# Performance work log

Measured on AMD Instinct MI355X. Metric: run time of the kernel, lower is better.

## Reference

```python
import jax, jax.numpy as jnp
import numpy as np

B, S, H, NH = 2, 2048, 1024, 16
HD = H // NH
INV_NORM = 1.0 / float(np.sqrt(HD))
BETA = 1.0


def setup_inputs() -> dict:
    key = jax.random.key(0)
    ks = jax.random.split(key, 8)
    causal = ~jnp.tril(jnp.ones((S, S), dtype=bool))  # True = masked (future)
    return {
        "hidden_states": jax.random.normal(ks[0], (B, S, H), dtype=jnp.float32),
        "residual": jax.random.normal(ks[1], (B, S, H), dtype=jnp.float32),
        "alibi": jax.random.normal(ks[2], (B * NH, 1, S), dtype=jnp.float32) * 0.1,
        "attention_mask": jnp.broadcast_to(causal[None, None], (B, 1, S, S)),
        "W_qkv": jax.random.normal(ks[3], (3 * H, H), dtype=jnp.float32) * (1.0 / np.sqrt(H)),
        "b_qkv": jax.random.normal(ks[4], (3 * H,), dtype=jnp.float32) * 0.02,
        "W_d": jax.random.normal(ks[5], (H, H), dtype=jnp.float32) * (1.0 / np.sqrt(H)),
        "b_d": jax.random.normal(ks[6], (H,), dtype=jnp.float32) * 0.02,
    }


def reference(hidden_states, residual, alibi, attention_mask, W_qkv, b_qkv, W_d, b_d):
    b, s, h = hidden_states.shape
    # fused QKV projection, split per-head interleaved [B,S,NH,3,HD]
    fused = hidden_states @ W_qkv.T + b_qkv
    fused = fused.reshape(b, s, NH, 3, HD)
    q = jnp.transpose(fused[..., 0, :], (0, 2, 1, 3))  # [B,NH,S,HD]
    k = jnp.transpose(fused[..., 1, :], (0, 2, 1, 3))
    v = jnp.transpose(fused[..., 2, :], (0, 2, 1, 3))
    # baddbmm: beta*alibi + alpha * q @ k^T
    scores = BETA * alibi.reshape(b, NH, 1, s) + INV_NORM * jnp.einsum(
        "bhqd,bhkd->bhqk", q, k
    )  # [B,NH,S,S]
    neg_min = jnp.finfo(scores.dtype).min
    scores = jnp.where(attention_mask, neg_min, scores)
    probs = jax.nn.softmax(scores.astype(jnp.float32), axis=-1).astype(scores.dtype)
    ctx = jnp.einsum("bhqk,bhkd->bhqd", probs, v)  # [B,NH,S,HD]
    ctx = jnp.transpose(ctx, (0, 2, 1, 3)).reshape(b, s, h)  # merge heads
    out = ctx @ W_d.T + b_d
    return residual + out  # dropout p=0
```

## Files before the change

kernel.cpp:

```cpp
#include <hip/hip_runtime.h>
#include <stdint.h>

#define BATCH 2
#define SLEN 2048
#define HDIM 1024
#define NH 16
#define HD 64
#define NHEADS 32
#define M_ROWS 4096
#define N_QKV 3072

typedef float f32x4 __attribute__((ext_vector_type(4)));
typedef float f32x16 __attribute__((ext_vector_type(16)));
typedef short bf16x8 __attribute__((ext_vector_type(8)));

typedef __attribute__((address_space(1))) unsigned int GU32;
typedef __attribute__((address_space(3))) unsigned int LU32;

__device__ __forceinline__ void gld16(const void* g, void* l) {
  __builtin_amdgcn_global_load_lds((GU32*)g, (LU32*)l, 16, 0, 0);
}

__device__ __forceinline__ unsigned short f2bf(float x) {
  union { float f; unsigned int u; } v; v.f = x;
  unsigned int r = v.u + 0x7fffu + ((v.u >> 16) & 1u);
  return (unsigned short)(r >> 16);
}

__device__ __forceinline__ float fexp2(float x) {
  float r; asm("v_exp_f32 %0, %1" : "=v"(r) : "v"(x)); return r;
}
__device__ __forceinline__ unsigned cvtpk(float lo, float hi) {
  unsigned r; asm("v_cvt_pk_bf16_f32 %0, %1, %2" : "=v"(r) : "v"(lo), "v"(hi)); return r;
}

#define MFMA32(a, b, c) __builtin_amdgcn_mfma_f32_32x32x16_bf16(a, b, c, 0, 0, 0)
#define MFMA16(a, b, c) __builtin_amdgcn_mfma_f32_16x16x32_bf16(a, b, c, 0, 0, 0)
#define ZERO16 {0.f,0.f,0.f,0.f,0.f,0.f,0.f,0.f,0.f,0.f,0.f,0.f,0.f,0.f,0.f,0.f}

__global__ void __launch_bounds__(256) k_prep(
    const float* __restrict__ hidden, const float* __restrict__ wqkv,
    const float* __restrict__ wd,
    unsigned short* __restrict__ hb, unsigned short* __restrict__ wqkb,
    unsigned short* __restrict__ wdb) {
  int bid = blockIdx.x;
  const float* src;
  unsigned short* dst;
  int i;
  if (bid < 4096)      { src = hidden; dst = hb;   i = bid * 256 + threadIdx.x; }
  else if (bid < 7168) { src = wqkv;  dst = wqkb;  i = (bid - 4096) * 256 + threadIdx.x; }
  else                 { src = wd;    dst = wdb;   i = (bid - 7168) * 256 + threadIdx.x; }
  float4 v = ((const float4*)src)[i];
  ushort4 o;
  o.x = f2bf(v.x); o.y = f2bf(v.y); o.z = f2bf(v.z); o.w = f2bf(v.w);
  ((ushort4*)dst)[i] = o;
}

__global__ void __launch_bounds__(256) k_gemm_qkv(
    const unsigned short* __restrict__ A,
    const unsigned short* __restrict__ Bw,
    const float* __restrict__ bias,
    unsigned short* __restrict__ Qo,
    unsigned short* __restrict__ Ko,
    unsigned short* __restrict__ Vto) {
  __shared__ __align__(16) unsigned short Alds[128 * 32];
  __shared__ __align__(16) unsigned short Blds[128 * 32];
  const int tid = threadIdx.x;
  const int w = tid >> 6, lane = tid & 63;
  const int g = lane >> 4, l15 = lane & 15;
  const int wr = w >> 1, wc = w & 1;
  const int tm = blockIdx.x * 128, tn = blockIdx.y * 128;

  const f32x4 zero = {0.f, 0.f, 0.f, 0.f};
  f32x4 acc[4][4];
#pragma unroll
  for (int m = 0; m < 4; ++m)
#pragma unroll
    for (int n = 0; n < 4; ++n) acc[m][n] = zero;

  for (int k0 = 0; k0 < 1024; k0 += 32) {
    __syncthreads();
#pragma unroll
    for (int r = 0; r < 2; ++r) {
      int c = r * 256 + w * 64 + lane;
      int row = c >> 2, cc = c & 3;
      gld16(A + (size_t)(tm + row) * 1024 + k0 + cc * 8,
            (char*)Alds + (r * 256 + w * 64) * 16);
      gld16(Bw + (size_t)(tn + row) * 1024 + k0 + cc * 8,
            (char*)Blds + (r * 256 + w * 64) * 16);
    }
    __syncthreads();
    bf16x8 af[4], bfv[4];
#pragma unroll
    for (int m = 0; m < 4; ++m)
      af[m] = *(const bf16x8*)(Alds + (wr * 64 + m * 16 + l15) * 32 + g * 8);
#pragma unroll
    for (int n = 0; n < 4; ++n)
      bfv[n] = *(const bf16x8*)(Blds + (wc * 64 + n * 16 + l15) * 32 + g * 8);
#pragma unroll
    for (int m = 0; m < 4; ++m)
#pragma unroll
      for (int n = 0; n < 4; ++n)
        acc[m][n] = MFMA16(af[m], bfv[n], acc[m][n]);
  }

#pragma unroll
  for (int n = 0; n < 4; ++n) {
    int col = tn + wc * 64 + n * 16 + l15;
    float bv = bias[col];
    int c6 = col >> 6;
    int nh = c6 / 3;
    int which = c6 - nh * 3;
    int hd = col & 63;
#pragma unroll
    for (int m = 0; m < 4; ++m) {
      int row0 = tm + wr * 64 + m * 16 + g * 4;
      int b = row0 >> 11;
      int s0 = row0 & 2047;
      int head = b * NH + nh;
      if (which == 2) {
        ushort4 pk;
        pk.x = f2bf(acc[m][n][0] + bv);
        pk.y = f2bf(acc[m][n][1] + bv);
        pk.z = f2bf(acc[m][n][2] + bv);
        pk.w = f2bf(acc[m][n][3] + bv);
        *(ushort4*)(Vto + ((size_t)head * HD + hd) * SLEN + s0) = pk;
      } else {
        unsigned short* dst = (which == 0) ? Qo : Ko;
        size_t base = (size_t)head * SLEN * HD;
#pragma unroll
        for (int j = 0; j < 4; ++j)
          dst[base + (size_t)(s0 + j) * HD + hd] = f2bf(acc[m][n][j] + bv);
      }
    }
  }
}

__global__ void __launch_bounds__(256) k_gemm_out(
    const unsigned short* __restrict__ A,
    const unsigned short* __restrict__ Bw,
    const float* __restrict__ bias,
    const float* __restrict__ residual,
    float* __restrict__ out) {
  __shared__ __align__(16) unsigned short Alds[128 * 32];
  __shared__ __align__(16) unsigned short Blds[64 * 32];
  const int tid = threadIdx.x;
  const int w = tid >> 6, lane = tid & 63;
  const int g = lane >> 4, l15 = lane & 15;
  const int wr = w >> 1, wc = w & 1;
  const int tm = blockIdx.x * 128, tn = blockIdx.y * 64;

  const f32x4 zero = {0.f, 0.f, 0.f, 0.f};
  f32x4 acc[4][2];
#pragma unroll
  for (int m = 0; m < 4; ++m)
#pragma unroll
    for (int n = 0; n < 2; ++n) acc[m][n] = zero;

  for (int k0 = 0; k0 < 1024; k0 += 32) {
    __syncthreads();
#pragma unroll
    for (int r = 0; r < 2; ++r) {
      int c = r * 256 + tid;
      int row = c >> 2, cc = c & 3;
      gld16(A + (size_t)(tm + row) * 1024 + k0 + cc * 8,
            (char*)Alds + c * 16);
    }
    {
      int row = tid >> 2, cc = tid & 3;
      gld16(Bw + (size_t)(tn + row) * 1024 + k0 + cc * 8,
            (char*)Blds + tid * 16);
    }
    __syncthreads();
    bf16x8 af[4], bfv[2];
#pragma unroll
    for (int m = 0; m < 4; ++m)
      af[m] = *(const bf16x8*)(Alds + (wr * 64 + m * 16 + l15) * 32 + g * 8);
#pragma unroll
    for (int n = 0; n < 2; ++n)
      bfv[n] = *(const bf16x8*)(Blds + (wc * 32 + n * 16 + l15) * 32 + g * 8);
#pragma unroll
    for (int m = 0; m < 4; ++m)
#pragma unroll
      for (int n = 0; n < 2; ++n)
        acc[m][n] = MFMA16(af[m], bfv[n], acc[m][n]);
  }

#pragma unroll
  for (int n = 0; n < 2; ++n) {
    int col = tn + wc * 32 + n * 16 + l15;
    float bv = bias[col];
#pragma unroll
    for (int m = 0; m < 4; ++m) {
      int row0 = tm + wr * 64 + m * 16 + g * 4;
#pragma unroll
      for (int j = 0; j < 4; ++j) {
        size_t idx = (size_t)(row0 + j) * 1024 + col;
        out[idx] = acc[m][n][j] + bv + residual[idx];
      }
    }
  }
}

__global__ void __launch_bounds__(512, 4) k_attn(
    const unsigned short* __restrict__ Q,
    const unsigned short* __restrict__ K,
    const unsigned short* __restrict__ Vt,
    const float* __restrict__ alibi,
    unsigned short* __restrict__ ctx) {
  __shared__ __align__(16) char Lbuf[40960];
  unsigned short* KlB = (unsigned short*)Lbuf;
  unsigned short* VlB = (unsigned short*)(Lbuf + 16384);
  float* Al = (float*)(Lbuf + 32768);

  const int n = blockIdx.x;
  const int head = n & 31;
  const int t = n >> 5;
  const int bq = (t < 8) ? (15 - t) : (t - 8);
  const int tid = threadIdx.x;
  const int w = tid >> 6, lane = tid & 63;
  const int l31 = lane & 31, h = lane >> 5;
  const int rsw = l31 & 7;
  const int qsub = w & 3, par = w >> 2;
  const int qw = bq * 128 + qsub * 32;
  const int ksd = 4 * bq + qsub;

  const unsigned short* Qh = Q + (size_t)head * SLEN * HD;
  const unsigned short* Kh = K + (size_t)head * SLEN * HD;
  const unsigned short* Vh = Vt + (size_t)head * HD * SLEN;

  bf16x8 qr0, qr1, qr2, qr3;
  {
    const unsigned short* qp = Qh + (size_t)(qw + l31) * HD + h * 8;
    qr0 = *(const bf16x8*)(qp);
    qr1 = *(const bf16x8*)(qp + 16);
    qr2 = *(const bf16x8*)(qp + 32);
    qr3 = *(const bf16x8*)(qp + 48);
  }

  f32x16 ot0 = ZERO16, ot1 = ZERO16;
  float m_run = -1e30f, l_acc = 0.f;
  const float C1 = 0.18033688011f;

#define STAGE(nb, itt)                                                          \
  do {                                                                          \
    const int kb_ = (itt) * 64;                                                 \
    const int row_ = tid >> 3;                                                  \
    const int sw_ = ((tid & 7) ^ (row_ & 7)) * 8;                               \
    gld16(Kh + (size_t)(kb_ + row_) * HD + sw_, (char*)(KlB + (nb) * 4096) + tid * 16); \
    gld16(Vh + (size_t)row_ * SLEN + kb_ + sw_, (char*)(VlB + (nb) * 4096) + tid * 16); \
  } while (0)

  STAGE(0, 0);
  {
    float4 av = *(const float4*)(alibi + (size_t)head * SLEN + tid * 4);
    av.x *= 1.44269504f; av.y *= 1.44269504f;
    av.z *= 1.44269504f; av.w *= 1.44269504f;
    *(float4*)(Al + tid * 4) = av;
  }
  __syncthreads();
  int cur = 0;
  const int itmax = 2 * bq + 2;

  for (int it = 0; it < itmax; ++it) {
    if (it + 1 < itmax) STAGE(cur ^ 1, it + 1);
    const int ks = 2 * it + par;
    if (ks <= ksd) {
      const char* kbase = (const char*)(KlB + cur * 4096);
      const char* vbase = (const char*)(VlB + cur * 4096);

      f32x16 st = ZERO16;
      __builtin_amdgcn_s_setprio(1);
      {
        const char* kr = kbase + (par * 32 + l31) * 128;
        st = MFMA32(*(const bf16x8*)(kr + (((0 + h) ^ rsw) * 16)), qr0, st);
        st = MFMA32(*(const bf16x8*)(kr + (((2 + h) ^ rsw) * 16)), qr1, st);
        st = MFMA32(*(const bf16x8*)(kr + (((4 + h) ^ rsw) * 16)), qr2, st);
        st = MFMA32(*(const bf16x8*)(kr + (((6 + h) ^ rsw) * 16)), qr3, st);
      }
      __builtin_amdgcn_s_setprio(0);

      const float* ab = Al + ks * 32 + 4 * h;
      f32x4 alq0 = *(const f32x4*)(ab);
      f32x4 alq1 = *(const f32x4*)(ab + 8);
      f32x4 alq2 = *(const f32x4*)(ab + 16);
      f32x4 alq3 = *(const f32x4*)(ab + 24);

      float p[16];
#pragma unroll
      for (int i = 0; i < 4; ++i) {
        p[i]      = st[i]      * C1 + alq0[i];
        p[4 + i]  = st[4 + i]  * C1 + alq1[i];
        p[8 + i]  = st[8 + i]  * C1 + alq2[i];
        p[12 + i] = st[12 + i] * C1 + alq3[i];
      }
      if (ks == ksd) {
#pragma unroll
        for (int i = 0; i < 16; ++i) {
          int krow = (i & 3) + 8 * (i >> 2) + 4 * h;
          p[i] = (krow > l31) ? -1e30f : p[i];
        }
      }
      float x0 = fmaxf(fmaxf(p[0], p[1]), p[2]);
      float x1 = fmaxf(fmaxf(p[3], p[4]), p[5]);
      float x2 = fmaxf(fmaxf(p[6], p[7]), p[8]);
      float x3 = fmaxf(fmaxf(p[9], p[10]), p[11]);
      float x4 = fmaxf(fmaxf(p[12], p[13]), p[14]);
      float pm = fmaxf(fmaxf(fmaxf(x0, x1), x2), fmaxf(fmaxf(x3, x4), p[15]));
      pm = fmaxf(pm, __shfl_xor(pm, 32));
      if (!__all(pm <= m_run + 8.0f)) {
        float mnew = fmaxf(m_run, pm);
        float sc = fexp2(m_run - mnew);
        m_run = mnew;
        l_acc *= sc;
        ot0 *= sc;
        ot1 *= sc;
      }
      float e[16];
      float ss = 0.f;
#pragma unroll
      for (int i = 0; i < 16; ++i) { e[i] = fexp2(p[i] - m_run); ss += e[i]; }
      l_acc += ss;

      unsigned a0 = cvtpk(e[0], e[1]),   a1 = cvtpk(e[2], e[3]);
      unsigned a2 = cvtpk(e[4], e[5]),   a3 = cvtpk(e[6], e[7]);
      unsigned b0 = cvtpk(e[8], e[9]),   b1 = cvtpk(e[10], e[11]);
      unsigned b2 = cvtpk(e[12], e[13]), b3 = cvtpk(e[14], e[15]);
      unsigned t0 = h ? a0 : a2, t1 = h ? a1 : a3;
      unsigned t2 = h ? b0 : b2, t3 = h ? b1 : b3;
      unsigned r0 = __shfl_xor(t0, 32), r1 = __shfl_xor(t1, 32);
      unsigned r2 = __shfl_xor(t2, 32), r3 = __shfl_xor(t3, 32);
      union { unsigned u[4]; bf16x8 v; } P0, P1;
      P0.u[0] = h ? r0 : a0;  P0.u[1] = h ? r1 : a1;
      P0.u[2] = h ? a2 : r0;  P0.u[3] = h ? a3 : r1;
      P1.u[0] = h ? r2 : b0;  P1.u[1] = h ? r3 : b1;
      P1.u[2] = h ? b2 : r2;  P1.u[3] = h ? b3 : r3;

      __builtin_amdgcn_s_setprio(1);
      {
        const char* vr0 = vbase + l31 * 128;
        const char* vr1 = vbase + (32 + l31) * 128;
        bf16x8 vf;
        vf = *(const bf16x8*)(vr0 + (((4 * par + 0 + h) ^ rsw) * 16)); ot0 = MFMA32(vf, P0.v, ot0);
        vf = *(const bf16x8*)(vr0 + (((4 * par + 2 + h) ^ rsw) * 16)); ot0 = MFMA32(vf, P1.v, ot0);
        vf = *(const bf16x8*)(vr1 + (((4 * par + 0 + h) ^ rsw) * 16)); ot1 = MFMA32(vf, P0.v, ot1);
        vf = *(const bf16x8*)(vr1 + (((4 * par + 2 + h) ^ rsw) * 16)); ot1 = MFMA32(vf, P1.v, ot1);
      }
      __builtin_amdgcn_s_setprio(0);
    }
    __syncthreads();
    cur ^= 1;
  }
#undef STAGE

  float* Ob = (float*)Lbuf;
  float* Mb = (float*)(Lbuf + 32768);
  const int idx = qsub * 64 + lane;
  const int xs = idx & 7;
  float* op = Ob + (size_t)idx * 32;
  if (par == 1) {
#pragma unroll
    for (int c = 0; c < 4; ++c) {
      f32x4 t2 = {ot0[4 * c], ot0[4 * c + 1], ot0[4 * c + 2], ot0[4 * c + 3]};
      *(f32x4*)(op + ((c ^ xs) * 4)) = t2;
      f32x4 u = {ot1[4 * c], ot1[4 * c + 1], ot1[4 * c + 2], ot1[4 * c + 3]};
      *(f32x4*)(op + (((c + 4) ^ xs) * 4)) = u;
    }
    Mb[idx * 2] = m_run;
    Mb[idx * 2 + 1] = l_acc;
  }
  __syncthreads();
  if (par == 0) {
    float m1 = Mb[idx * 2], l1 = Mb[idx * 2 + 1];
    float mt = fmaxf(m_run, m1);
    float s0 = fexp2(m_run - mt), s1 = fexp2(m1 - mt);
    float lme = l_acc * s0 + l1 * s1;
    float ltot = lme + __shfl_xor(lme, 32);
    float inv = 1.0f / ltot;
#pragma unroll
    for (int c = 0; c < 4; ++c) {
      f32x4 t2 = *(const f32x4*)(op + ((c ^ xs) * 4));
      f32x4 u = *(const f32x4*)(op + (((c + 4) ^ xs) * 4));
#pragma unroll
      for (int j = 0; j < 4; ++j) {
        ot0[4 * c + j] = ot0[4 * c + j] * s0 + t2[j] * s1;
        ot1[4 * c + j] = ot1[4 * c + j] * s0 + u[j] * s1;
      }
    }
    const int b = head >> 4, nh = head & 15;
    unsigned short* cb = ctx + ((size_t)b * SLEN + qw + l31) * HDIM + nh * HD + 4 * h;
#pragma unroll
    for (int rg = 0; rg < 4; ++rg) {
      ushort4 o;
      o.x = f2bf(ot0[4 * rg + 0] * inv);
      o.y = f2bf(ot0[4 * rg + 1] * inv);
      o.z = f2bf(ot0[4 * rg + 2] * inv);
      o.w = f2bf(ot0[4 * rg + 3] * inv);
      *(ushort4*)(cb + 8 * rg) = o;
      o.x = f2bf(ot1[4 * rg + 0] * inv);
      o.y = f2bf(ot1[4 * rg + 1] * inv);
      o.z = f2bf(ot1[4 * rg + 2] * inv);
      o.w = f2bf(ot1[4 * rg + 3] * inv);
      *(ushort4*)(cb + 32 + 8 * rg) = o;
    }
  }
}

extern "C" void kernel_launch(void* const* d_in, const int* in_sizes, int n_in,
                              void* d_out, int out_size, void* d_ws, size_t ws_size,
                              hipStream_t stream) {
  const float* hidden   = (const float*)d_in[0];
  const float* residual = (const float*)d_in[1];
  const float* alibi    = (const float*)d_in[2];
  const float* W_qkv = (const float*)d_in[4];
  const float* b_qkv = (const float*)d_in[5];
  const float* W_d   = (const float*)d_in[6];
  const float* b_d   = (const float*)d_in[7];
  float* out = (float*)d_out;

  unsigned short* hb   = (unsigned short*)d_ws;
  unsigned short* wqkb = hb + (size_t)M_ROWS * HDIM;
  unsigned short* wdb  = wqkb + (size_t)N_QKV * HDIM;
  unsigned short* Qb   = wdb + (size_t)HDIM * HDIM;
  unsigned short* Kb   = Qb + (size_t)NHEADS * SLEN * HD;
  unsigned short* Vtb  = Kb + (size_t)NHEADS * SLEN * HD;
  unsigned short* ctxb = Vtb + (size_t)NHEADS * SLEN * HD;

  k_prep<<<dim3(8192), dim3(256), 0, stream>>>(hidden, W_qkv, W_d, hb, wqkb, wdb);
  k_gemm_qkv<<<dim3(32, 24), dim3(256), 0, stream>>>(hb, wqkb, b_qkv, Qb, Kb, Vtb);
  k_attn<<<dim3(512), dim3(512), 0, stream>>>(Qb, Kb, Vtb, alibi, ctxb);
  k_gemm_out<<<dim3(32, 16), dim3(256), 0, stream>>>(ctxb, wdb, b_d, residual, out);
}
```

Before: 103.0 us.

## Fuse fp32-to-bf16 conversion into GEMM tile loads and drop prep kernel

Removes the separate conversion kernel and has both GEMMs load fp32 activations and weights directly into LDS, converting to bf16 in registers before the MFMAs. LDS tiles use an XOR swizzle to avoid bank conflicts on the wider fp32 rows. This removes a kernel launch and the full read/write pass through the bf16 staging buffers. In exchange, each GEMM moves twice the bytes per tile from memory and LDS, and repeats the conversion for every tile that reuses the same data.

```diff
diff --git a/kernel.cpp b/kernel.cpp
--- a/kernel.cpp
+++ b/kernel.cpp
@@ -38,33 +38,24 @@
 #define MFMA16(a, b, c) __builtin_amdgcn_mfma_f32_16x16x32_bf16(a, b, c, 0, 0, 0)
 #define ZERO16 {0.f,0.f,0.f,0.f,0.f,0.f,0.f,0.f,0.f,0.f,0.f,0.f,0.f,0.f,0.f,0.f}
 
-__global__ void __launch_bounds__(256) k_prep(
-    const float* __restrict__ hidden, const float* __restrict__ wqkv,
-    const float* __restrict__ wd,
-    unsigned short* __restrict__ hb, unsigned short* __restrict__ wqkb,
-    unsigned short* __restrict__ wdb) {
-  int bid = blockIdx.x;
-  const float* src;
-  unsigned short* dst;
-  int i;
-  if (bid < 4096)      { src = hidden; dst = hb;   i = bid * 256 + threadIdx.x; }
-  else if (bid < 7168) { src = wqkv;  dst = wqkb;  i = (bid - 4096) * 256 + threadIdx.x; }
-  else                 { src = wd;    dst = wdb;   i = (bid - 7168) * 256 + threadIdx.x; }
-  float4 v = ((const float4*)src)[i];
-  ushort4 o;
-  o.x = f2bf(v.x); o.y = f2bf(v.y); o.z = f2bf(v.z); o.w = f2bf(v.w);
-  ((ushort4*)dst)[i] = o;
+__device__ __forceinline__ bf16x8 pack8(f32x4 lo, f32x4 hi) {
+  union { unsigned u[4]; bf16x8 v; } P;
+  P.u[0] = cvtpk(lo[0], lo[1]);
+  P.u[1] = cvtpk(lo[2], lo[3]);
+  P.u[2] = cvtpk(hi[0], hi[1]);
+  P.u[3] = cvtpk(hi[2], hi[3]);
+  return P.v;
 }
 
 __global__ void __launch_bounds__(256) k_gemm_qkv(
-    const unsigned short* __restrict__ A,
-    const unsigned short* __restrict__ Bw,
+    const float* __restrict__ A,
+    const float* __restrict__ Bw,
     const float* __restrict__ bias,
     unsigned short* __restrict__ Qo,
     unsigned short* __restrict__ Ko,
     unsigned short* __restrict__ Vto) {
-  __shared__ __align__(16) unsigned short Alds[128 * 32];
-  __shared__ __align__(16) unsigned short Blds[128 * 32];
+  __shared__ __align__(16) float Alds[128 * 32];
+  __shared__ __align__(16) float Blds[128 * 32];
   const int tid = threadIdx.x;
   const int w = tid >> 6, lane = tid & 63;
   const int g = lane >> 4, l15 = lane & 15;
@@ -81,22 +72,33 @@
   for (int k0 = 0; k0 < 1024; k0 += 32) {
     __syncthreads();
 #pragma unroll
-    for (int r = 0; r < 2; ++r) {
-      int c = r * 256 + w * 64 + lane;
-      int row = c >> 2, cc = c & 3;
-      gld16(A + (size_t)(tm + row) * 1024 + k0 + cc * 8,
-            (char*)Alds + (r * 256 + w * 64) * 16);
-      gld16(Bw + (size_t)(tn + row) * 1024 + k0 + cc * 8,
-            (char*)Blds + (r * 256 + w * 64) * 16);
+    for (int r = 0; r < 4; ++r) {
+      int c = r * 256 + tid;
+      int row = c >> 3, cc = c & 7;
+      int ccs = cc ^ (row & 7);
+      gld16(A + (size_t)(tm + row) * 1024 + k0 + ccs * 4, (char*)Alds + c * 16);
+      gld16(Bw + (size_t)(tn + row) * 1024 + k0 + ccs * 4, (char*)Blds + c * 16);
     }
     __syncthreads();
     bf16x8 af[4], bfv[4];
 #pragma unroll
-    for (int m = 0; m < 4; ++m)
-      af[m] = *(const bf16x8*)(Alds + (wr * 64 + m * 16 + l15) * 32 + g * 8);
-#pragma unroll
-    for (int n = 0; n < 4; ++n)
-      bfv[n] = *(const bf16x8*)(Blds + (wc * 64 + n * 16 + l15) * 32 + g * 8);
+    for (int m = 0; m < 4; ++m) {
+      int row = wr * 64 + m * 16 + l15;
+      int sw = row & 7;
+      const float* ar = Alds + row * 32;
+      f32x4 lo = *(const f32x4*)(ar + (((g * 2) ^ sw) * 4));
+      f32x4 hi = *(const f32x4*)(ar + (((g * 2 + 1) ^ sw) * 4));
+      af[m] = pack8(lo, hi);
+    }
+#pragma unroll
+    for (int n = 0; n < 4; ++n) {
+      int row = wc * 64 + n * 16 + l15;
+      int sw = row & 7;
+      const float* br = Blds + row * 32;
+      f32x4 lo = *(const f32x4*)(br + (((g * 2) ^ sw) * 4));
+      f32x4 hi = *(const f32x4*)(br + (((g * 2 + 1) ^ sw) * 4));
+      bfv[n] = pack8(lo, hi);
+    }
 #pragma unroll
     for (int m = 0; m < 4; ++m)
 #pragma unroll
@@ -138,12 +140,12 @@
 
 __global__ void __launch_bounds__(256) k_gemm_out(
     const unsigned short* __restrict__ A,
-    const unsigned short* __restrict__ Bw,
+    const float* __restrict__ Bw,
     const float* __restrict__ bias,
     const float* __restrict__ residual,
     float* __restrict__ out) {
   __shared__ __align__(16) unsigned short Alds[128 * 32];
-  __shared__ __align__(16) unsigned short Blds[64 * 32];
+  __shared__ __align__(16) float Blds[64 * 32];
   const int tid = threadIdx.x;
   const int w = tid >> 6, lane = tid & 63;
   const int g = lane >> 4, l15 = lane & 15;
@@ -166,10 +168,12 @@
       gld16(A + (size_t)(tm + row) * 1024 + k0 + cc * 8,
             (char*)Alds + c * 16);
     }
-    {
-      int row = tid >> 2, cc = tid & 3;
-      gld16(Bw + (size_t)(tn + row) * 1024 + k0 + cc * 8,
-            (char*)Blds + tid * 16);
+#pragma unroll
+    for (int r = 0; r < 2; ++r) {
+      int c = r * 256 + tid;
+      int row = c >> 3, cc = c & 7;
+      int ccs = cc ^ (row & 7);
+      gld16(Bw + (size_t)(tn + row) * 1024 + k0 + ccs * 4, (char*)Blds + c * 16);
     }
     __syncthreads();
     bf16x8 af[4], bfv[2];
@@ -177,8 +181,14 @@
     for (int m = 0; m < 4; ++m)
       af[m] = *(const bf16x8*)(Alds + (wr * 64 + m * 16 + l15) * 32 + g * 8);
 #pragma unroll
-    for (int n = 0; n < 2; ++n)
-      bfv[n] = *(const bf16x8*)(Blds + (wc * 32 + n * 16 + l15) * 32 + g * 8);
+    for (int n = 0; n < 2; ++n) {
+      int row = wc * 32 + n * 16 + l15;
+      int sw = row & 7;
+      const float* br = Blds + row * 32;
+      f32x4 lo = *(const f32x4*)(br + (((g * 2) ^ sw) * 4));
+      f32x4 hi = *(const f32x4*)(br + (((g * 2 + 1) ^ sw) * 4));
+      bfv[n] = pack8(lo, hi);
+    }
 #pragma unroll
     for (int m = 0; m < 4; ++m)
 #pragma unroll
@@ -418,16 +428,12 @@
   const float* b_d   = (const float*)d_in[7];
   float* out = (float*)d_out;
 
-  unsigned short* hb   = (unsigned short*)d_ws;
-  unsigned short* wqkb = hb + (size_t)M_ROWS * HDIM;
-  unsigned short* wdb  = wqkb + (size_t)N_QKV * HDIM;
-  unsigned short* Qb   = wdb + (size_t)HDIM * HDIM;
+  unsigned short* Qb   = (unsigned short*)d_ws;
   unsigned short* Kb   = Qb + (size_t)NHEADS * SLEN * HD;
   unsigned short* Vtb  = Kb + (size_t)NHEADS * SLEN * HD;
   unsigned short* ctxb = Vtb + (size_t)NHEADS * SLEN * HD;
 
-  k_prep<<<dim3(8192), dim3(256), 0, stream>>>(hidden, W_qkv, W_d, hb, wqkb, wdb);
-  k_gemm_qkv<<<dim3(32, 24), dim3(256), 0, stream>>>(hb, wqkb, b_qkv, Qb, Kb, Vtb);
+  k_gemm_qkv<<<dim3(32, 24), dim3(256), 0, stream>>>(hidden, W_qkv, b_qkv, Qb, Kb, Vtb);
   k_attn<<<dim3(512), dim3(512), 0, stream>>>(Qb, Kb, Vtb, alibi, ctxb);
-  k_gemm_out<<<dim3(32, 16), dim3(256), 0, stream>>>(ctxb, wdb, b_d, residual, out);
-}
+  k_gemm_out<<<dim3(32, 16), dim3(256), 0, stream>>>(ctxb, W_d, b_d, residual, out);
+}
```

After: 117.9 us. 1.14x slower.
